# Kernel tuning notes

Measured on AMD Instinct MI355X. Metric: run time of the kernel, lower is better.

## Reference

```python
import jax, jax.numpy as jnp
import numpy as np

NOISE_SIGMA = 0.005
P_DROPOUT = 0.003125
P_RANDOM = 0.003125
P_STICK = 0.00025

B, H, W = 64, 480, 640
DS = 4


def setup_inputs() -> dict:
    key = jax.random.key(0)
    ks = jax.random.split(key, 12)
    return {
        "depth": jax.random.uniform(ks[0], (B, 1, H, W), dtype=jnp.float32),
        "noise_lo": jax.random.normal(ks[1], (B, 1, H // DS, W // DS), dtype=jnp.float32),
        "dropout_u": jax.random.uniform(ks[2], (B, 1, H, W), dtype=jnp.float32),
        "random_u": jax.random.uniform(ks[3], (B, 1, H, W), dtype=jnp.float32),
        "random_vals": jax.random.uniform(ks[4], (B, 1, H, W), dtype=jnp.float32),
        "stick_u": jax.random.uniform(ks[5], (B,), dtype=jnp.float32),
        "horiz_u": jax.random.uniform(ks[6], (B,), dtype=jnp.float32),
        "fallback_vals": jax.random.uniform(ks[7], (B,), dtype=jnp.float32),
        "stick_len": jax.random.randint(ks[8], (B,), 0, 18, dtype=jnp.int32),
        "stick_width": jax.random.randint(ks[9], (B,), 0, 3, dtype=jnp.int32),
        "stick_y": jax.random.randint(ks[10], (B,), 0, H, dtype=jnp.int32),
        "stick_x": jax.random.randint(ks[11], (B,), 0, W, dtype=jnp.int32),
    }


def reference(depth, noise_lo, dropout_u, random_u, random_vals,
              stick_u, horiz_u, fallback_vals,
              stick_len, stick_width, stick_y, stick_x):
    b, c, h, w = depth.shape
    # 1. correlated spatial noise: bilinear upsample (half-pixel centers ==
    #    torch align_corners=False)
    noise = jax.image.resize(noise_lo * NOISE_SIGMA, (b, 1, h, w), method="bilinear")
    valid = (depth > 0).astype(depth.dtype)
    depth = jnp.clip(depth + noise * valid, 0.0, 1.0)
    # 2. pixel dropout
    depth = depth * (dropout_u >= P_DROPOUT).astype(depth.dtype)
    # 3. random value insertion
    depth = jnp.where(random_u < P_RANDOM, random_vals, depth)
    # 4. stick artifacts (one stick per selected sample, vectorized)
    stick_on = stick_u < P_STICK * h * w                      # [B]
    horizontal = horiz_u > 0.5                                # [B]
    length = stick_len + 1                                    # 1..max_stick_len
    width = stick_width + 1                                   # 1..max_stick_width
    span_h = jnp.where(horizontal, width, length)             # rows covered
    span_w = jnp.where(horizontal, length, width)             # cols covered
    y = jnp.clip(stick_y, 0, jnp.maximum(h - span_h, 1) - 1)
    x = jnp.clip(stick_x, 0, jnp.maximum(w - span_w, 1) - 1)
    dval = depth[jnp.arange(b), 0, y, x]                      # anchor pixel value
    val = jnp.where(dval > 0, dval, fallback_vals)            # [B]
    rows = jnp.arange(h)[None, :, None]                       # [1,H,1]
    cols = jnp.arange(w)[None, None, :]                       # [1,1,W]
    y_ = y[:, None, None]
    x_ = x[:, None, None]
    mask = ((rows >= y_) & (rows < y_ + span_h[:, None, None]) &
            (cols >= x_) & (cols < x_ + span_w[:, None, None]) &
            stick_on[:, None, None])                          # [B,H,W]
    depth = jnp.where(mask[:, None, :, :], val[:, None, None, None], depth)
    return depth
```

## Files before the change

### kernel.cpp

```cpp
#include <hip/hip_runtime.h>


constexpr int Bc  = 64;
constexpr int Hc  = 480;
constexpr int Wc  = 640;
constexpr int HLO = 120;
constexpr int WLO = 160;
constexpr int W4  = Wc / 4;
constexpr int HW  = Hc * Wc;

#define NOISE_SIGMA 0.005f
#define P_DROPOUT   0.003125f
#define P_RANDOM    0.003125f
#define STICK_THRESH 76.8f

__global__ __launch_bounds__(256) void aug_main_kernel(
    const float* __restrict__ depth,
    const float* __restrict__ noise_lo,
    const float* __restrict__ dropout_u,
    const float* __restrict__ random_u,
    const float* __restrict__ random_vals,
    float* __restrict__ out)
{
    const int b = blockIdx.y;
    const int t = blockIdx.x * 256 + threadIdx.x;
    const int y = t / W4;
    const int c = t - y * W4;

    const int r = y & 3, k = y >> 2;
    const int y0 = (r < 2) ? (k - 1) : k;
    const float fy = (r == 0) ? 0.625f : (r == 1) ? 0.875f : (r == 2) ? 0.125f : 0.375f;
    const float gy = 1.0f - fy;
    const int ya = max(y0, 0);
    const int yb = min(y0 + 1, HLO - 1);

    const float* lo = noise_lo + (size_t)b * (HLO * WLO);
    const int xm = max(c - 1, 0);
    const int xp = min(c + 1, WLO - 1);
    const float* la = lo + ya * WLO;
    const float* lb = lo + yb * WLO;
    const float v0 = la[xm] * gy + lb[xm] * fy;
    const float v1 = la[c]  * gy + lb[c]  * fy;
    const float v2 = la[xp] * gy + lb[xp] * fy;

    const float n0 = (v0 * 0.375f + v1 * 0.625f) * NOISE_SIGMA;
    const float n1 = (v0 * 0.125f + v1 * 0.875f) * NOISE_SIGMA;
    const float n2 = (v1 * 0.875f + v2 * 0.125f) * NOISE_SIGMA;
    const float n3 = (v1 * 0.625f + v2 * 0.375f) * NOISE_SIGMA;

    const size_t idx = (size_t)b * HW + (size_t)t * 4;
    const float4 d  = *reinterpret_cast<const float4*>(depth     + idx);
    const float4 du = *reinterpret_cast<const float4*>(dropout_u + idx);
    const float4 ru = *reinterpret_cast<const float4*>(random_u  + idx);

    float o0 = fminf(fmaxf(d.x + (d.x > 0.0f ? n0 : 0.0f), 0.0f), 1.0f);
    float o1 = fminf(fmaxf(d.y + (d.y > 0.0f ? n1 : 0.0f), 0.0f), 1.0f);
    float o2 = fminf(fmaxf(d.z + (d.z > 0.0f ? n2 : 0.0f), 0.0f), 1.0f);
    float o3 = fminf(fmaxf(d.w + (d.w > 0.0f ? n3 : 0.0f), 0.0f), 1.0f);

    if (du.x < P_DROPOUT) o0 = 0.0f;
    if (du.y < P_DROPOUT) o1 = 0.0f;
    if (du.z < P_DROPOUT) o2 = 0.0f;
    if (du.w < P_DROPOUT) o3 = 0.0f;

    if (ru.x < P_RANDOM) o0 = random_vals[idx + 0];
    if (ru.y < P_RANDOM) o1 = random_vals[idx + 1];
    if (ru.z < P_RANDOM) o2 = random_vals[idx + 2];
    if (ru.w < P_RANDOM) o3 = random_vals[idx + 3];

    *reinterpret_cast<float4*>(out + idx) = make_float4(o0, o1, o2, o3);
}

__global__ __launch_bounds__(64) void stick_kernel(
    const float* __restrict__ stick_u,
    const float* __restrict__ horiz_u,
    const float* __restrict__ fallback_vals,
    const int* __restrict__ stick_len,
    const int* __restrict__ stick_width,
    const int* __restrict__ stick_y,
    const int* __restrict__ stick_x,
    float* __restrict__ out)
{
    const int b = blockIdx.x;
    if (!(stick_u[b] < STICK_THRESH)) return;

    const bool horizontal = horiz_u[b] > 0.5f;
    const int length = stick_len[b] + 1;
    const int width  = stick_width[b] + 1;
    const int span_h = horizontal ? width : length;
    const int span_w = horizontal ? length : width;
    const int ymax = max(Hc - span_h, 1) - 1;
    const int xmax = max(Wc - span_w, 1) - 1;
    const int y = min(max(stick_y[b], 0), ymax);
    const int x = min(max(stick_x[b], 0), xmax);

    float* outb = out + (size_t)b * HW;
    const float dval = outb[y * Wc + x];
    const float val = (dval > 0.0f) ? dval : fallback_vals[b];
    __syncthreads();

    const int total = span_h * span_w;
    for (int i = threadIdx.x; i < total; i += 64) {
        const int rr = i / span_w;
        const int cc = i - rr * span_w;
        outb[(y + rr) * Wc + (x + cc)] = val;
    }
}

extern "C" void kernel_launch(void* const* d_in, const int* in_sizes, int n_in,
                              void* d_out, int out_size, void* d_ws, size_t ws_size,
                              hipStream_t stream) {
    const float* depth       = (const float*)d_in[0];
    const float* noise_lo    = (const float*)d_in[1];
    const float* dropout_u   = (const float*)d_in[2];
    const float* random_u    = (const float*)d_in[3];
    const float* random_vals = (const float*)d_in[4];
    const float* stick_u     = (const float*)d_in[5];
    const float* horiz_u     = (const float*)d_in[6];
    const float* fallback    = (const float*)d_in[7];
    const int*   slen        = (const int*)d_in[8];
    const int*   swid        = (const int*)d_in[9];
    const int*   sy          = (const int*)d_in[10];
    const int*   sx          = (const int*)d_in[11];
    float* out = (float*)d_out;

    dim3 grid(Hc * W4 / 256, Bc);
    aug_main_kernel<<<grid, 256, 0, stream>>>(depth, noise_lo, dropout_u,
                                              random_u, random_vals, out);
    stick_kernel<<<Bc, 64, 0, stream>>>(stick_u, horiz_u, fallback,
                                        slen, swid, sy, sx, out);
}
```

Baseline: 299.6 us.

## Fuse stick kernel into main pass, process 16 pixels per thread with nontemporal I/O

Folds the stick-artifact pass into the main augmentation kernel: each thread recomputes the anchor pixel's augmented value from the inputs and overwrites its own outputs where they fall inside the stick rectangle, so the second launch goes away. Each thread now handles four float4 chunks spaced 160 columns apart, which issues more independent loads per thread and lowers the thread count. Loads and stores use nontemporal builtins to avoid polluting the cache on a streaming workload. Costs are higher register pressure and the anchor value being recomputed by every thread on the stick rows.

```diff
diff --git a/kernel.cpp b/kernel.cpp
--- a/kernel.cpp
+++ b/kernel.cpp
@@ -1,18 +1,25 @@
 #include <hip/hip_runtime.h>
 
+
+typedef float f32x4 __attribute__((ext_vector_type(4)));
 
 constexpr int Bc  = 64;
 constexpr int Hc  = 480;
 constexpr int Wc  = 640;
 constexpr int HLO = 120;
 constexpr int WLO = 160;
-constexpr int W4  = Wc / 4;
 constexpr int HW  = Hc * Wc;
+constexpr int CS  = 40;
 
 #define NOISE_SIGMA 0.005f
 #define P_DROPOUT   0.003125f
 #define P_RANDOM    0.003125f
 #define STICK_THRESH 76.8f
+
+__device__ __forceinline__ float vlerp(const float* la, const float* lb,
+                                       int col, float gy, float fy) {
+    return la[col] * gy + lb[col] * fy;
+}
 
 __global__ __launch_bounds__(256) void aug_main_kernel(
     const float* __restrict__ depth,
@@ -20,58 +27,6 @@
     const float* __restrict__ dropout_u,
     const float* __restrict__ random_u,
     const float* __restrict__ random_vals,
-    float* __restrict__ out)
-{
-    const int b = blockIdx.y;
-    const int t = blockIdx.x * 256 + threadIdx.x;
-    const int y = t / W4;
-    const int c = t - y * W4;
-
-    const int r = y & 3, k = y >> 2;
-    const int y0 = (r < 2) ? (k - 1) : k;
-    const float fy = (r == 0) ? 0.625f : (r == 1) ? 0.875f : (r == 2) ? 0.125f : 0.375f;
-    const float gy = 1.0f - fy;
-    const int ya = max(y0, 0);
-    const int yb = min(y0 + 1, HLO - 1);
-
-    const float* lo = noise_lo + (size_t)b * (HLO * WLO);
-    const int xm = max(c - 1, 0);
-    const int xp = min(c + 1, WLO - 1);
-    const float* la = lo + ya * WLO;
-    const float* lb = lo + yb * WLO;
-    const float v0 = la[xm] * gy + lb[xm] * fy;
-    const float v1 = la[c]  * gy + lb[c]  * fy;
-    const float v2 = la[xp] * gy + lb[xp] * fy;
-
-    const float n0 = (v0 * 0.375f + v1 * 0.625f) * NOISE_SIGMA;
-    const float n1 = (v0 * 0.125f + v1 * 0.875f) * NOISE_SIGMA;
-    const float n2 = (v1 * 0.875f + v2 * 0.125f) * NOISE_SIGMA;
-    const float n3 = (v1 * 0.625f + v2 * 0.375f) * NOISE_SIGMA;
-
-    const size_t idx = (size_t)b * HW + (size_t)t * 4;
-    const float4 d  = *reinterpret_cast<const float4*>(depth     + idx);
-    const float4 du = *reinterpret_cast<const float4*>(dropout_u + idx);
-    const float4 ru = *reinterpret_cast<const float4*>(random_u  + idx);
-
-    float o0 = fminf(fmaxf(d.x + (d.x > 0.0f ? n0 : 0.0f), 0.0f), 1.0f);
-    float o1 = fminf(fmaxf(d.y + (d.y > 0.0f ? n1 : 0.0f), 0.0f), 1.0f);
-    float o2 = fminf(fmaxf(d.z + (d.z > 0.0f ? n2 : 0.0f), 0.0f), 1.0f);
-    float o3 = fminf(fmaxf(d.w + (d.w > 0.0f ? n3 : 0.0f), 0.0f), 1.0f);
-
-    if (du.x < P_DROPOUT) o0 = 0.0f;
-    if (du.y < P_DROPOUT) o1 = 0.0f;
-    if (du.z < P_DROPOUT) o2 = 0.0f;
-    if (du.w < P_DROPOUT) o3 = 0.0f;
-
-    if (ru.x < P_RANDOM) o0 = random_vals[idx + 0];
-    if (ru.y < P_RANDOM) o1 = random_vals[idx + 1];
-    if (ru.z < P_RANDOM) o2 = random_vals[idx + 2];
-    if (ru.w < P_RANDOM) o3 = random_vals[idx + 3];
-
-    *reinterpret_cast<float4*>(out + idx) = make_float4(o0, o1, o2, o3);
-}
-
-__global__ __launch_bounds__(64) void stick_kernel(
     const float* __restrict__ stick_u,
     const float* __restrict__ horiz_u,
     const float* __restrict__ fallback_vals,
@@ -81,30 +36,135 @@
     const int* __restrict__ stick_x,
     float* __restrict__ out)
 {
-    const int b = blockIdx.x;
-    if (!(stick_u[b] < STICK_THRESH)) return;
+    const int b = blockIdx.y;
+    const int t = blockIdx.x * 256 + threadIdx.x;
+    const int y = t / CS;
+    const int c = t - y * CS;
 
-    const bool horizontal = horiz_u[b] > 0.5f;
-    const int length = stick_len[b] + 1;
-    const int width  = stick_width[b] + 1;
-    const int span_h = horizontal ? width : length;
-    const int span_w = horizontal ? length : width;
-    const int ymax = max(Hc - span_h, 1) - 1;
-    const int xmax = max(Wc - span_w, 1) - 1;
-    const int y = min(max(stick_y[b], 0), ymax);
-    const int x = min(max(stick_x[b], 0), xmax);
+    const int r = y & 3, k = y >> 2;
+    const int y0 = (r < 2) ? (k - 1) : k;
+    const float fy = (r == 0) ? 0.625f : (r == 1) ? 0.875f : (r == 2) ? 0.125f : 0.375f;
+    const float gy = 1.0f - fy;
+    const int ya = max(y0, 0);
+    const int yb = min(y0 + 1, HLO - 1);
 
-    float* outb = out + (size_t)b * HW;
-    const float dval = outb[y * Wc + x];
-    const float val = (dval > 0.0f) ? dval : fallback_vals[b];
-    __syncthreads();
+    const size_t base = (size_t)b * HW + (size_t)y * Wc;
+    const size_t iA = base + (size_t)c * 4;
+    const size_t iB = iA + 160;
+    const size_t iC = iA + 320;
+    const size_t iD = iA + 480;
 
-    const int total = span_h * span_w;
-    for (int i = threadIdx.x; i < total; i += 64) {
-        const int rr = i / span_w;
-        const int cc = i - rr * span_w;
-        outb[(y + rr) * Wc + (x + cc)] = val;
+    const f32x4 dA = __builtin_nontemporal_load(reinterpret_cast<const f32x4*>(depth     + iA));
+    const f32x4 dB = __builtin_nontemporal_load(reinterpret_cast<const f32x4*>(depth     + iB));
+    const f32x4 dC = __builtin_nontemporal_load(reinterpret_cast<const f32x4*>(depth     + iC));
+    const f32x4 dD = __builtin_nontemporal_load(reinterpret_cast<const f32x4*>(depth     + iD));
+    const f32x4 uA = __builtin_nontemporal_load(reinterpret_cast<const f32x4*>(dropout_u + iA));
+    const f32x4 uB = __builtin_nontemporal_load(reinterpret_cast<const f32x4*>(dropout_u + iB));
+    const f32x4 uC = __builtin_nontemporal_load(reinterpret_cast<const f32x4*>(dropout_u + iC));
+    const f32x4 uD = __builtin_nontemporal_load(reinterpret_cast<const f32x4*>(dropout_u + iD));
+    const f32x4 rA = __builtin_nontemporal_load(reinterpret_cast<const f32x4*>(random_u  + iA));
+    const f32x4 rB = __builtin_nontemporal_load(reinterpret_cast<const f32x4*>(random_u  + iB));
+    const f32x4 rC = __builtin_nontemporal_load(reinterpret_cast<const f32x4*>(random_u  + iC));
+    const f32x4 rD = __builtin_nontemporal_load(reinterpret_cast<const f32x4*>(random_u  + iD));
+
+    const float* lo = noise_lo + (size_t)b * (HLO * WLO);
+    const float* la = lo + ya * WLO;
+    const float* lb = lo + yb * WLO;
+    const float a0 = vlerp(la, lb, max(c - 1, 0), gy, fy);
+    const float a1 = vlerp(la, lb, c,             gy, fy);
+    const float a2 = vlerp(la, lb, c + 1,         gy, fy);
+    const float b0 = vlerp(la, lb, c + 39,        gy, fy);
+    const float b1 = vlerp(la, lb, c + 40,        gy, fy);
+    const float b2 = vlerp(la, lb, c + 41,        gy, fy);
+    const float c0 = vlerp(la, lb, c + 79,        gy, fy);
+    const float c1 = vlerp(la, lb, c + 80,        gy, fy);
+    const float c2 = vlerp(la, lb, c + 81,        gy, fy);
+    const float d0 = vlerp(la, lb, c + 119,       gy, fy);
+    const float d1 = vlerp(la, lb, c + 120,       gy, fy);
+    const float d2 = vlerp(la, lb, min(c + 121, WLO - 1), gy, fy);
+
+#define HN(p0, p1, p2, n0, n1, n2, n3)                         \
+    const float n0 = (p0 * 0.375f + p1 * 0.625f) * NOISE_SIGMA; \
+    const float n1 = (p0 * 0.125f + p1 * 0.875f) * NOISE_SIGMA; \
+    const float n2 = (p1 * 0.875f + p2 * 0.125f) * NOISE_SIGMA; \
+    const float n3 = (p1 * 0.625f + p2 * 0.375f) * NOISE_SIGMA;
+    HN(a0, a1, a2, nA0, nA1, nA2, nA3)
+    HN(b0, b1, b2, nB0, nB1, nB2, nB3)
+    HN(c0, c1, c2, nC0, nC1, nC2, nC3)
+    HN(d0, d1, d2, nD0, nD1, nD2, nD3)
+#undef HN
+
+#define AUG(dv, uv, rv, n0, n1, n2, n3, idx, q0, q1, q2, q3)                  \
+    float q0 = fminf(fmaxf(dv.x + (dv.x > 0.0f ? n0 : 0.0f), 0.0f), 1.0f);    \
+    float q1 = fminf(fmaxf(dv.y + (dv.y > 0.0f ? n1 : 0.0f), 0.0f), 1.0f);    \
+    float q2 = fminf(fmaxf(dv.z + (dv.z > 0.0f ? n2 : 0.0f), 0.0f), 1.0f);    \
+    float q3 = fminf(fmaxf(dv.w + (dv.w > 0.0f ? n3 : 0.0f), 0.0f), 1.0f);    \
+    if (uv.x < P_DROPOUT) q0 = 0.0f;                                          \
+    if (uv.y < P_DROPOUT) q1 = 0.0f;                                          \
+    if (uv.z < P_DROPOUT) q2 = 0.0f;                                          \
+    if (uv.w < P_DROPOUT) q3 = 0.0f;                                          \
+    if (rv.x < P_RANDOM) q0 = random_vals[idx + 0];                           \
+    if (rv.y < P_RANDOM) q1 = random_vals[idx + 1];                           \
+    if (rv.z < P_RANDOM) q2 = random_vals[idx + 2];                           \
+    if (rv.w < P_RANDOM) q3 = random_vals[idx + 3];
+    AUG(dA, uA, rA, nA0, nA1, nA2, nA3, iA, oA0, oA1, oA2, oA3)
+    AUG(dB, uB, rB, nB0, nB1, nB2, nB3, iB, oB0, oB1, oB2, oB3)
+    AUG(dC, uC, rC, nC0, nC1, nC2, nC3, iC, oC0, oC1, oC2, oC3)
+    AUG(dD, uD, rD, nD0, nD1, nD2, nD3, iD, oD0, oD1, oD2, oD3)
+#undef AUG
+
+    if (stick_u[b] < STICK_THRESH) {
+        const bool horizontal = horiz_u[b] > 0.5f;
+        const int length = stick_len[b] + 1;
+        const int width  = stick_width[b] + 1;
+        const int sh = horizontal ? width : length;
+        const int sw = horizontal ? length : width;
+        const int ry = min(max(stick_y[b], 0), max(Hc - sh, 1) - 1);
+        const int rx = min(max(stick_x[b], 0), max(Wc - sw, 1) - 1);
+        if (y >= ry && y < ry + sh) {
+            const size_t pi = (size_t)b * HW + (size_t)ry * Wc + rx;
+            float dv = depth[pi];
+            {
+                const int vr = ry & 3, vk = ry >> 2;
+                const int vy0 = (vr < 2) ? (vk - 1) : vk;
+                const float vfy = (vr == 0) ? 0.625f : (vr == 1) ? 0.875f : (vr == 2) ? 0.125f : 0.375f;
+                const int vya = max(vy0, 0), vyb = min(vy0 + 1, HLO - 1);
+                const int hg = rx >> 2, hr = rx & 3;
+                const int hx0 = (hr < 2) ? (hg - 1) : hg;
+                const float wfx = (hr == 0) ? 0.625f : (hr == 1) ? 0.875f : (hr == 2) ? 0.125f : 0.375f;
+                const int hxa = max(hx0, 0), hxb = min(hx0 + 1, WLO - 1);
+                const float nlo = lo[vya * WLO + hxa] * (1.0f - vfy) + lo[vyb * WLO + hxa] * vfy;
+                const float nhi = lo[vya * WLO + hxb] * (1.0f - vfy) + lo[vyb * WLO + hxb] * vfy;
+                const float nz = (nlo * (1.0f - wfx) + nhi * wfx) * NOISE_SIGMA;
+                dv = fminf(fmaxf(dv + (dv > 0.0f ? nz : 0.0f), 0.0f), 1.0f);
+            }
+            if (dropout_u[pi] < P_DROPOUT) dv = 0.0f;
+            if (random_u[pi]  < P_RANDOM)  dv = random_vals[pi];
+            const float val = (dv > 0.0f) ? dv : fallback_vals[b];
+
+            const int xlo = rx, xhi = rx + sw;
+#define APPLY(colbase, q0, q1, q2, q3)                                \
+            { const int cb = (colbase);                               \
+              if (cb + 0 >= xlo && cb + 0 < xhi) q0 = val;            \
+              if (cb + 1 >= xlo && cb + 1 < xhi) q1 = val;            \
+              if (cb + 2 >= xlo && cb + 2 < xhi) q2 = val;            \
+              if (cb + 3 >= xlo && cb + 3 < xhi) q3 = val; }
+            APPLY(c * 4,        oA0, oA1, oA2, oA3)
+            APPLY(c * 4 + 160,  oB0, oB1, oB2, oB3)
+            APPLY(c * 4 + 320,  oC0, oC1, oC2, oC3)
+            APPLY(c * 4 + 480,  oD0, oD1, oD2, oD3)
+#undef APPLY
+        }
     }
+
+    f32x4 oA; oA.x = oA0; oA.y = oA1; oA.z = oA2; oA.w = oA3;
+    f32x4 oB; oB.x = oB0; oB.y = oB1; oB.z = oB2; oB.w = oB3;
+    f32x4 oC; oC.x = oC0; oC.y = oC1; oC.z = oC2; oC.w = oC3;
+    f32x4 oD; oD.x = oD0; oD.y = oD1; oD.z = oD2; oD.w = oD3;
+    __builtin_nontemporal_store(oA, reinterpret_cast<f32x4*>(out + iA));
+    __builtin_nontemporal_store(oB, reinterpret_cast<f32x4*>(out + iB));
+    __builtin_nontemporal_store(oC, reinterpret_cast<f32x4*>(out + iC));
+    __builtin_nontemporal_store(oD, reinterpret_cast<f32x4*>(out + iD));
 }
 
 extern "C" void kernel_launch(void* const* d_in, const int* in_sizes, int n_in,
@@ -124,9 +184,9 @@
     const int*   sx          = (const int*)d_in[11];
     float* out = (float*)d_out;
 
-    dim3 grid(Hc * W4 / 256, Bc);
+    dim3 grid(Hc * CS / 256, Bc);
     aug_main_kernel<<<grid, 256, 0, stream>>>(depth, noise_lo, dropout_u,
-                                              random_u, random_vals, out);
-    stick_kernel<<<Bc, 64, 0, stream>>>(stick_u, horiz_u, fallback,
-                                        slen, swid, sy, sx, out);
+                                              random_u, random_vals,
+                                              stick_u, horiz_u, fallback,
+                                              slen, swid, sy, sx, out);
 }
```

Result: faster. 279.6 us (-6.7%).
